# Performance work log

Hardware: AMD Instinct MI355X
Metric: run time of the kernel (lower is better)

## Reference

```python
import jax, jax.numpy as jnp
import numpy as np

EMB_DIM = 1024
N_HEAD = 16
HEAD_DIM = EMB_DIM // N_HEAD


def setup_inputs() -> dict:
    key = jax.random.key(0)
    k1, k2, k3, k4, k5 = jax.random.split(key, 5)
    x = jax.random.normal(k1, (4, 2048, EMB_DIM), dtype=jnp.float32)
    s = 1.0 / np.sqrt(EMB_DIM)
    W_qkv = jax.random.uniform(k2, (3 * EMB_DIM, EMB_DIM), minval=-s, maxval=s, dtype=jnp.float32)
    b_qkv = jax.random.uniform(k3, (3 * EMB_DIM,), minval=-s, maxval=s, dtype=jnp.float32)
    W_proj = jax.random.uniform(k4, (EMB_DIM, EMB_DIM), minval=-s, maxval=s, dtype=jnp.float32)
    b_proj = jax.random.uniform(k5, (EMB_DIM,), minval=-s, maxval=s, dtype=jnp.float32)
    return {"x": x, "W_qkv": W_qkv, "b_qkv": b_qkv, "W_proj": W_proj, "b_proj": b_proj}


def reference(x, W_qkv, b_qkv, W_proj, b_proj):
    B, S, E = x.shape
    H, D = N_HEAD, HEAD_DIM
    qkv = x @ W_qkv.T + b_qkv  # [B,S,3E]
    q, k, v = jnp.split(qkv, 3, axis=-1)
    # [B,S,E] -> [B,H,S,D]
    q = q.reshape(B, S, H, D).transpose(0, 2, 1, 3)
    k = k.reshape(B, S, H, D).transpose(0, 2, 1, 3)
    v = v.reshape(B, S, H, D).transpose(0, 2, 1, 3)
    scale = 1.0 / jnp.sqrt(jnp.asarray(D, dtype=x.dtype))
    scores = jnp.einsum('bhqd,bhkd->bhqk', q, k) * scale
    causal = jnp.tril(jnp.ones((S, S), dtype=bool))
    scores = jnp.where(causal, scores, jnp.asarray(-jnp.inf, dtype=scores.dtype))
    attn = jax.nn.softmax(scores, axis=-1)
    y = jnp.einsum('bhqk,bhkd->bhqd', attn, v)  # [B,H,S,D]
    y = y.transpose(0, 2, 1, 3).reshape(B, S, E)
    return y @ W_proj.T + b_proj
```

## Files before the change

kernel.cpp:

```cpp
#include <hip/hip_runtime.h>
#include <hip/hip_bf16.h>

typedef __attribute__((ext_vector_type(4))) float f32x4;
typedef __attribute__((ext_vector_type(8))) __bf16 bf16x8;
typedef __attribute__((ext_vector_type(4))) unsigned int u32x4;

#define EMB 1024
#define NHEAD 16
#define HDIM 64
#define SEQ 2048
#define BATCH 4
#define NTOK 8192

__device__ __forceinline__ unsigned short f2bf(float f) {
    unsigned int u = __builtin_bit_cast(unsigned int, f);
    u = (u + 0x7fffu + ((u >> 16) & 1u)) >> 16;
    return (unsigned short)u;
}

__device__ __forceinline__ unsigned int pack_bf2(float lo, float hi) {
    unsigned int a = __builtin_bit_cast(unsigned int, lo);
    unsigned int b = __builtin_bit_cast(unsigned int, hi);
    return ((a + 0x8000u) >> 16) | ((b + 0x8000u) & 0xffff0000u);
}

__device__ __forceinline__ unsigned long long pack_bf4(const f32x4 v) {
    unsigned long long lo = pack_bf2(v[0], v[1]);
    unsigned long long hi = pack_bf2(v[2], v[3]);
    return (hi << 32) | lo;
}

__device__ __forceinline__ void async_copy16(const ushort* g, ushort* l) {
    __builtin_amdgcn_global_load_lds(
        (const __attribute__((address_space(1))) void*)g,
        (__attribute__((address_space(3))) void*)l,
        16, 0, 0);
}

__global__ void cvt_f32_bf16(const float4* __restrict__ in, ushort* __restrict__ out, int n4) {
    int i = blockIdx.x * 256 + threadIdx.x;
    if (i < n4) {
        float4 v = in[i];
        ushort4 o;
        o.x = f2bf(v.x); o.y = f2bf(v.y); o.z = f2bf(v.z); o.w = f2bf(v.w);
        ((ushort4*)out)[i] = o;
    }
}

#define GEMM_STAGE(Asrc, Bsrc, m0, n0, kt)                                        \
    {                                                                             \
        _Pragma("unroll")                                                         \
        for (int j = 0; j < 2; ++j) {                                             \
            int row = wave * 32 + j * 16 + (lane >> 2);                           \
            int kc  = (lane & 3) ^ ((row >> 1) & 3);                              \
            async_copy16(Asrc + (size_t)(m0 + row) * EMB + kt + kc * 8,           \
                         As + (wave * 32 + j * 16) * 32);                         \
            async_copy16(Bsrc + (size_t)(n0 + row) * EMB + kt + kc * 8,           \
                         Bs + (wave * 32 + j * 16) * 32);                         \
        }                                                                         \
    }

#define GEMM_BODY(Asrc, Bsrc, m0, n0)                                             \
    f32x4 acc[4][4] = {};                                                         \
    for (int kt = 0; kt < EMB; kt += 32) {                                        \
        GEMM_STAGE(Asrc, Bsrc, m0, n0, kt)                                        \
        __syncthreads();                                                          \
        bf16x8 a[4], b[4];                                                        \
        _Pragma("unroll")                                                         \
        for (int i = 0; i < 4; ++i) {                                             \
            int r = wm + i * 16 + col;                                            \
            a[i] = *(const bf16x8*)&As[r * 32 + (quad ^ ((r >> 1) & 3)) * 8];     \
            int c = wn + i * 16 + col;                                            \
            b[i] = *(const bf16x8*)&Bs[c * 32 + (quad ^ ((c >> 1) & 3)) * 8];     \
        }                                                                         \
        _Pragma("unroll")                                                         \
        for (int i = 0; i < 4; ++i)                                               \
            _Pragma("unroll")                                                     \
            for (int j = 0; j < 4; ++j)                                           \
                acc[i][j] = __builtin_amdgcn_mfma_f32_16x16x32_bf16(              \
                    a[i], b[j], acc[i][j], 0, 0, 0);                              \
        __syncthreads();                                                         \
    }

__global__ __launch_bounds__(256) void gemm_qk(
    const ushort* __restrict__ A,
    const ushort* __restrict__ W,
    const float*  __restrict__ bias,
    ushort* __restrict__ Qb, ushort* __restrict__ Kb)
{
    __shared__ ushort As[128 * 32];
    __shared__ ushort Bs[128 * 32];
    const int tid  = threadIdx.x;
    const int lane = tid & 63;
    const int wave = tid >> 6;
    const int col  = lane & 15;
    const int quad = lane >> 4;
    const int m0 = blockIdx.x * 128;
    const int n0 = blockIdx.y * 128;
    const int wm = (wave >> 1) * 64;
    const int wn = (wave & 1) * 64;

    GEMM_BODY(A, W, m0, n0)

    #pragma unroll
    for (int i = 0; i < 4; ++i)
        #pragma unroll
        for (int j = 0; j < 4; ++j)
            #pragma unroll
            for (int r = 0; r < 4; ++r) {
                int m = m0 + wm + i * 16 + quad * 4 + r;
                int n = n0 + wn + j * 16 + col;
                float v = acc[i][j][r] + bias[n];
                unsigned short bv = f2bf(v);
                int e = n & 1023;
                int h = e >> 6, d = e & 63;
                int b = m >> 11, s = m & 2047;
                size_t bh = (size_t)(b * NHEAD + h);
                if (n < 1024) Qb[(bh * SEQ + s) * HDIM + d] = bv;
                else          Kb[(bh * SEQ + s) * HDIM + d] = bv;
            }
}

__global__ __launch_bounds__(256) void gemm_vt(
    const ushort* __restrict__ Wv,
    const ushort* __restrict__ X,
    const float*  __restrict__ bias,
    ushort* __restrict__ Vtx)
{
    __shared__ ushort As[128 * 32];
    __shared__ ushort Bs[128 * 32];
    const int tid  = threadIdx.x;
    const int lane = tid & 63;
    const int wave = tid >> 6;
    const int col  = lane & 15;
    const int quad = lane >> 4;
    const int m0 = blockIdx.x * 128;
    const int n0 = blockIdx.y * 128;
    const int wm = (wave >> 1) * 64;
    const int wn = (wave & 1) * 64;

    GEMM_BODY(Wv, X, m0, n0)

    #pragma unroll
    for (int i = 0; i < 4; ++i)
        #pragma unroll
        for (int j = 0; j < 4; ++j)
            #pragma unroll
            for (int r = 0; r < 4; ++r) {
                int m = m0 + wm + i * 16 + quad * 4 + r;
                int n = n0 + wn + j * 16 + col;
                Vtx[(size_t)m * NTOK + n] = f2bf(acc[i][j][r] + bias[m]);
            }
}

__global__ __launch_bounds__(256) void gemm_proj(
    const ushort* __restrict__ A,
    const ushort* __restrict__ W,
    const float*  __restrict__ bias,
    float* __restrict__ out)
{
    __shared__ ushort As[128 * 32];
    __shared__ ushort Bs[128 * 32];
    const int tid  = threadIdx.x;
    const int lane = tid & 63;
    const int wave = tid >> 6;
    const int col  = lane & 15;
    const int quad = lane >> 4;
    const int m0 = blockIdx.x * 128;
    const int n0 = blockIdx.y * 128;
    const int wm = (wave >> 1) * 64;
    const int wn = (wave & 1) * 64;

    GEMM_BODY(A, W, m0, n0)

    #pragma unroll
    for (int i = 0; i < 4; ++i)
        #pragma unroll
        for (int j = 0; j < 4; ++j)
            #pragma unroll
            for (int r = 0; r < 4; ++r) {
                int m = m0 + wm + i * 16 + quad * 4 + r;
                int n = n0 + wn + j * 16 + col;
                out[(size_t)m * EMB + n] = acc[i][j][r] + bias[n];
            }
}

__device__ __forceinline__ void attn_qtile(
    int qt, int b, int h, int lane, int wave,
    const ushort* __restrict__ Qh, const ushort* __restrict__ Kh,
    const ushort* __restrict__ Vh, ushort* __restrict__ Yb,
    ushort* __restrict__ Ks0, ushort* __restrict__ Ks1, ushort* __restrict__ Vs,
    ushort* __restrict__ Ps)
{
    const int col  = lane & 15;
    const int quad = lane >> 4;
    const int q0   = qt * 128 + wave * 32;
    const float SC = 0.125f * 1.44269504f;

    bf16x8 qf[2][2];
    #pragma unroll
    for (int g = 0; g < 2; ++g) {
        const ushort* qp = Qh + (size_t)(q0 + g * 16 + col) * HDIM;
        qf[g][0] = *(const bf16x8*)(qp + quad * 8);
        qf[g][1] = *(const bf16x8*)(qp + 32 + quad * 8);
    }

    ushort* Pw = Ps + wave * 4096;

    f32x4 o[2][4] = {};
    float lrun[2] = {0.f, 0.f};

    const int nk = qt + 1;
    for (int kt = 0; kt < nk; ++kt) {
        const int k0 = kt * 128;
        const bool last = (kt == nk - 1);

        {
            int srow = wave * 16 + (lane >> 2);
            #pragma unroll
            for (int rr = 0; rr < 2; ++rr) {
                int r = rr * 64 + srow;
                int kc = (lane & 3) ^ ((r >> 1) & 3);
                const ushort* src = Kh + (size_t)(k0 + r) * HDIM + kc * 8;
                async_copy16(src,      Ks0 + (rr * 64 + wave * 16) * 32);
                async_copy16(src + 32, Ks1 + (rr * 64 + wave * 16) * 32);
            }
            int kc = (lane & 3) ^ ((srow >> 1) & 3);
            const ushort* vsrc = Vh + (size_t)srow * NTOK + k0 + kc * 8;
            #pragma unroll
            for (int kq = 0; kq < 4; ++kq)
                async_copy16(vsrc + kq * 32, Vs + kq * 2048 + (wave * 16) * 32);
        }
        __syncthreads();

        f32x4 st[2][8];
        #pragma unroll
        for (int j = 0; j < 8; ++j) {
            int r = j * 16 + col;
            int q_ = (quad ^ ((r >> 1) & 3)) * 8;
            bf16x8 kf0 = *(const bf16x8*)&Ks0[r * 32 + q_];
            bf16x8 kf1 = *(const bf16x8*)&Ks1[r * 32 + q_];
            #pragma unroll
            for (int g = 0; g < 2; ++g) {
                f32x4 z = {0.f, 0.f, 0.f, 0.f};
                f32x4 t = __builtin_amdgcn_mfma_f32_16x16x32_bf16(kf0, qf[g][0], z, 0, 0, 0);
                st[g][j] = __builtin_amdgcn_mfma_f32_16x16x32_bf16(kf1, qf[g][1], t, 0, 0, 0);
            }
        }

        #pragma unroll
        for (int g = 0; g < 2; ++g) {
            int rowg = q0 + g * 16 + col;
            #pragma unroll
            for (int j = 0; j < 8; ++j)
                #pragma unroll
                for (int r = 0; r < 4; ++r) {
                    float pv = exp2f(st[g][j][r] * SC);
                    if (last) {
                        int c = k0 + j * 16 + quad * 4 + r;
                        pv = (c <= rowg) ? pv : 0.f;
                    }
                    st[g][j][r] = pv;
                    lrun[g] += pv;
                }
        }

        #pragma unroll
        for (int g = 0; g < 2; ++g)
            #pragma unroll
            for (int j = 0; j < 8; ++j) {
                int blk = 2 * j + (quad >> 1);
                *(unsigned long long*)&Pw[g * 2048 + col * 128 +
                                          ((blk ^ col) & 15) * 8 + (quad & 1) * 4]
                    = pack_bf4(st[g][j]);
            }
        bf16x8 pf[2][4];
        #pragma unroll
        for (int g = 0; g < 2; ++g)
            #pragma unroll
            for (int kq = 0; kq < 4; ++kq) {
                int blk = 4 * kq + quad;
                pf[g][kq] = *(const bf16x8*)&Pw[g * 2048 + col * 128 +
                                                ((blk ^ col) & 15) * 8];
            }

        #pragma unroll
        for (int dt = 0; dt < 4; ++dt) {
            int r = dt * 16 + col;
            int q_ = (quad ^ ((r >> 1) & 3)) * 8;
            #pragma unroll
            for (int kq = 0; kq < 4; ++kq) {
                bf16x8 vf = *(const bf16x8*)&Vs[kq * 2048 + r * 32 + q_];
                o[0][dt] = __builtin_amdgcn_mfma_f32_16x16x32_bf16(vf, pf[0][kq], o[0][dt], 0, 0, 0);
                o[1][dt] = __builtin_amdgcn_mfma_f32_16x16x32_bf16(vf, pf[1][kq], o[1][dt], 0, 0, 0);
            }
        }
        __syncthreads();
    }

    #pragma unroll
    for (int g = 0; g < 2; ++g) {
        float l = lrun[g];
        l += __shfl_xor(l, 16, 64);
        l += __shfl_xor(l, 32, 64);
        float inv = 1.f / l;
        int rowg = q0 + g * 16 + col;
        size_t rbase = ((size_t)(b * SEQ + rowg)) * EMB + h * HDIM + quad * 4;
        #pragma unroll
        for (int dt = 0; dt < 4; ++dt) {
            ushort4 s4;
            s4.x = f2bf(o[g][dt][0] * inv);
            s4.y = f2bf(o[g][dt][1] * inv);
            s4.z = f2bf(o[g][dt][2] * inv);
            s4.w = f2bf(o[g][dt][3] * inv);
            *(ushort4*)(Yb + rbase + dt * 16) = s4;
        }
    }
}

__global__ __launch_bounds__(256, 2) void attn(
    const ushort* __restrict__ Qb, const ushort* __restrict__ Kb,
    const ushort* __restrict__ Vtx, ushort* __restrict__ Yb)
{
    __shared__ ushort Ks0[128 * 32];
    __shared__ ushort Ks1[128 * 32];
    __shared__ ushort Vs[4 * 64 * 32];
    __shared__ __align__(16) ushort Ps[4 * 4096];
    const int lane = threadIdx.x & 63;
    const int wave = threadIdx.x >> 6;
    const int bh   = blockIdx.x & 63;
    const int pr   = blockIdx.x >> 6;

    const int b = bh >> 4, h = bh & 15;
    const ushort* Qh = Qb + (size_t)bh * SEQ * HDIM;
    const ushort* Kh = Kb + (size_t)bh * SEQ * HDIM;
    const ushort* Vh = Vtx + (size_t)(h * HDIM) * NTOK + b * SEQ;

    attn_qtile(15 - pr, b, h, lane, wave, Qh, Kh, Vh, Yb, Ks0, Ks1, Vs, Ps);
    __syncthreads();
    attn_qtile(pr,      b, h, lane, wave, Qh, Kh, Vh, Yb, Ks0, Ks1, Vs, Ps);
}

extern "C" void kernel_launch(void* const* d_in, const int* in_sizes, int n_in,
                              void* d_out, int out_size, void* d_ws, size_t ws_size,
                              hipStream_t stream) {
    const float* x      = (const float*)d_in[0];
    const float* W_qkv  = (const float*)d_in[1];
    const float* b_qkv  = (const float*)d_in[2];
    const float* W_proj = (const float*)d_in[3];
    const float* b_proj = (const float*)d_in[4];
    float* out = (float*)d_out;

    ushort* ws     = (ushort*)d_ws;
    ushort* Xb     = ws;
    ushort* Yb     = ws;
    ushort* Wqkvb  = ws + 8388608;
    ushort* Wprojb = ws + 11534336;
    ushort* Qb     = ws + 12582912;
    ushort* Kb     = ws + 20971520;
    ushort* Vtx    = ws + 29360128;

    cvt_f32_bf16<<<8192, 256, 0, stream>>>((const float4*)x,      Xb,     2097152);
    cvt_f32_bf16<<<3072, 256, 0, stream>>>((const float4*)W_qkv,  Wqkvb,  786432);
    cvt_f32_bf16<<<1024, 256, 0, stream>>>((const float4*)W_proj, Wprojb, 262144);

    gemm_qk<<<dim3(64, 16), 256, 0, stream>>>(Xb, Wqkvb, b_qkv, Qb, Kb);
    gemm_vt<<<dim3(8, 64), 256, 0, stream>>>(Wqkvb + (size_t)2048 * EMB, Xb,
                                             b_qkv + 2048, Vtx);
    attn<<<512, 256, 0, stream>>>(Qb, Kb, Vtx, Yb);
    gemm_proj<<<dim3(64, 8), 256, 0, stream>>>(Yb, Wprojb, b_proj, out);
}
```

Baseline: 269.5 us.

## Deepen GEMM K-step, shrink attention P buffer, raise occupancy, use hardware bf16 cvt

The GEMMs now stage 64 K-columns per barrier pair in two half buffers, halving the number of syncs and issuing more async loads per stage. The attention kernel splits the softmax exp loop into masked and unmasked paths and uses the raw hardware exp2. It reuses one P scratch slice per wave for both row groups, halving shared memory so that occupancy can be raised to 3 blocks per CU. bf16 packing switches to the compiler's native conversion, which rounds to nearest-even instead of rounding half up. The GEMMs use twice the LDS, and the tighter launch bounds may cause register spills.

```diff
diff --git a/kernel.cpp b/kernel.cpp
--- a/kernel.cpp
+++ b/kernel.cpp
@@ -18,16 +18,16 @@
     return (unsigned short)u;
 }
 
-__device__ __forceinline__ unsigned int pack_bf2(float lo, float hi) {
-    unsigned int a = __builtin_bit_cast(unsigned int, lo);
-    unsigned int b = __builtin_bit_cast(unsigned int, hi);
-    return ((a + 0x8000u) >> 16) | ((b + 0x8000u) & 0xffff0000u);
+__device__ __forceinline__ unsigned int cvt2_bf16(float lo, float hi) {
+    unsigned short a = __builtin_bit_cast(unsigned short, (__bf16)lo);
+    unsigned short b = __builtin_bit_cast(unsigned short, (__bf16)hi);
+    return (unsigned int)a | ((unsigned int)b << 16);
 }
 
 __device__ __forceinline__ unsigned long long pack_bf4(const f32x4 v) {
-    unsigned long long lo = pack_bf2(v[0], v[1]);
-    unsigned long long hi = pack_bf2(v[2], v[3]);
-    return (hi << 32) | lo;
+    unsigned long long lo = cvt2_bf16(v[0], v[1]);
+    unsigned long long hi = cvt2_bf16(v[2], v[3]);
+    return lo | (hi << 32);
 }
 
 __device__ __forceinline__ void async_copy16(const ushort* g, ushort* l) {
@@ -47,39 +47,46 @@
     }
 }
 
-#define GEMM_STAGE(Asrc, Bsrc, m0, n0, kt)                                        \
+#define GEMM_STAGE64(Asrc, Bsrc, m0, n0, kt)                                      \
     {                                                                             \
         _Pragma("unroll")                                                         \
         for (int j = 0; j < 2; ++j) {                                             \
             int row = wave * 32 + j * 16 + (lane >> 2);                           \
             int kc  = (lane & 3) ^ ((row >> 1) & 3);                              \
-            async_copy16(Asrc + (size_t)(m0 + row) * EMB + kt + kc * 8,           \
-                         As + (wave * 32 + j * 16) * 32);                         \
-            async_copy16(Bsrc + (size_t)(n0 + row) * EMB + kt + kc * 8,           \
-                         Bs + (wave * 32 + j * 16) * 32);                         \
+            const ushort* asrc = Asrc + (size_t)(m0 + row) * EMB + kt + kc * 8;   \
+            const ushort* bsrc = Bsrc + (size_t)(n0 + row) * EMB + kt + kc * 8;   \
+            async_copy16(asrc,      As0 + (wave * 32 + j * 16) * 32);             \
+            async_copy16(asrc + 32, As1 + (wave * 32 + j * 16) * 32);             \
+            async_copy16(bsrc,      Bs0 + (wave * 32 + j * 16) * 32);             \
+            async_copy16(bsrc + 32, Bs1 + (wave * 32 + j * 16) * 32);             \
         }                                                                         \
     }
 
-#define GEMM_BODY(Asrc, Bsrc, m0, n0)                                             \
+#define GEMM_BODY64(Asrc, Bsrc, m0, n0)                                           \
     f32x4 acc[4][4] = {};                                                         \
-    for (int kt = 0; kt < EMB; kt += 32) {                                        \
-        GEMM_STAGE(Asrc, Bsrc, m0, n0, kt)                                        \
+    for (int kt = 0; kt < EMB; kt += 64) {                                        \
+        GEMM_STAGE64(Asrc, Bsrc, m0, n0, kt)                                      \
         __syncthreads();                                                          \
-        bf16x8 a[4], b[4];                                                        \
         _Pragma("unroll")                                                         \
-        for (int i = 0; i < 4; ++i) {                                             \
-            int r = wm + i * 16 + col;                                            \
-            a[i] = *(const bf16x8*)&As[r * 32 + (quad ^ ((r >> 1) & 3)) * 8];     \
-            int c = wn + i * 16 + col;                                            \
-            b[i] = *(const bf16x8*)&Bs[c * 32 + (quad ^ ((c >> 1) & 3)) * 8];     \
+        for (int hf = 0; hf < 2; ++hf) {                                          \
+            const ushort* Ah = hf ? As1 : As0;                                    \
+            const ushort* Bh = hf ? Bs1 : Bs0;                                    \
+            bf16x8 a[4], b[4];                                                    \
+            _Pragma("unroll")                                                     \
+            for (int i = 0; i < 4; ++i) {                                         \
+                int r = wm + i * 16 + col;                                        \
+                a[i] = *(const bf16x8*)&Ah[r * 32 + (quad ^ ((r >> 1) & 3)) * 8]; \
+                int c = wn + i * 16 + col;                                        \
+                b[i] = *(const bf16x8*)&Bh[c * 32 + (quad ^ ((c >> 1) & 3)) * 8]; \
+            }                                                                     \
+            _Pragma("unroll")                                                     \
+            for (int i = 0; i < 4; ++i)                                           \
+                _Pragma("unroll")                                                 \
+                for (int j = 0; j < 4; ++j)                                       \
+                    acc[i][j] = __builtin_amdgcn_mfma_f32_16x16x32_bf16(          \
+                        a[i], b[j], acc[i][j], 0, 0, 0);                          \
         }                                                                         \
-        _Pragma("unroll")                                                         \
-        for (int i = 0; i < 4; ++i)                                               \
-            _Pragma("unroll")                                                     \
-            for (int j = 0; j < 4; ++j)                                           \
-                acc[i][j] = __builtin_amdgcn_mfma_f32_16x16x32_bf16(              \
-                    a[i], b[j], acc[i][j], 0, 0, 0);                              \
-        __syncthreads();                                                         \
+        __syncthreads();                                                          \
     }
 
 __global__ __launch_bounds__(256) void gemm_qk(
@@ -88,8 +95,10 @@
     const float*  __restrict__ bias,
     ushort* __restrict__ Qb, ushort* __restrict__ Kb)
 {
-    __shared__ ushort As[128 * 32];
-    __shared__ ushort Bs[128 * 32];
+    __shared__ ushort As0[128 * 32];
+    __shared__ ushort As1[128 * 32];
+    __shared__ ushort Bs0[128 * 32];
+    __shared__ ushort Bs1[128 * 32];
     const int tid  = threadIdx.x;
     const int lane = tid & 63;
     const int wave = tid >> 6;
@@ -100,7 +109,7 @@
     const int wm = (wave >> 1) * 64;
     const int wn = (wave & 1) * 64;
 
-    GEMM_BODY(A, W, m0, n0)
+    GEMM_BODY64(A, W, m0, n0)
 
     #pragma unroll
     for (int i = 0; i < 4; ++i)
@@ -127,8 +136,10 @@
     const float*  __restrict__ bias,
     ushort* __restrict__ Vtx)
 {
-    __shared__ ushort As[128 * 32];
-    __shared__ ushort Bs[128 * 32];
+    __shared__ ushort As0[128 * 32];
+    __shared__ ushort As1[128 * 32];
+    __shared__ ushort Bs0[128 * 32];
+    __shared__ ushort Bs1[128 * 32];
     const int tid  = threadIdx.x;
     const int lane = tid & 63;
     const int wave = tid >> 6;
@@ -139,7 +150,7 @@
     const int wm = (wave >> 1) * 64;
     const int wn = (wave & 1) * 64;
 
-    GEMM_BODY(Wv, X, m0, n0)
+    GEMM_BODY64(Wv, X, m0, n0)
 
     #pragma unroll
     for (int i = 0; i < 4; ++i)
@@ -159,8 +170,10 @@
     const float*  __restrict__ bias,
     float* __restrict__ out)
 {
-    __shared__ ushort As[128 * 32];
-    __shared__ ushort Bs[128 * 32];
+    __shared__ ushort As0[128 * 32];
+    __shared__ ushort As1[128 * 32];
+    __shared__ ushort Bs0[128 * 32];
+    __shared__ ushort Bs1[128 * 32];
     const int tid  = threadIdx.x;
     const int lane = tid & 63;
     const int wave = tid >> 6;
@@ -171,7 +184,7 @@
     const int wm = (wave >> 1) * 64;
     const int wn = (wave & 1) * 64;
 
-    GEMM_BODY(A, W, m0, n0)
+    GEMM_BODY64(A, W, m0, n0)
 
     #pragma unroll
     for (int i = 0; i < 4; ++i)
@@ -205,7 +218,7 @@
         qf[g][1] = *(const bf16x8*)(qp + 32 + quad * 8);
     }
 
-    ushort* Pw = Ps + wave * 4096;
+    ushort* Pw = Ps + wave * 2048;
 
     f32x4 o[2][4] = {};
     float lrun[2] = {0.f, 0.f};
@@ -248,41 +261,49 @@
             }
         }
 
-        #pragma unroll
-        for (int g = 0; g < 2; ++g) {
-            int rowg = q0 + g * 16 + col;
-            #pragma unroll
-            for (int j = 0; j < 8; ++j)
+        if (last) {
+            #pragma unroll
+            for (int g = 0; g < 2; ++g) {
+                int rowg = q0 + g * 16 + col;
                 #pragma unroll
-                for (int r = 0; r < 4; ++r) {
-                    float pv = exp2f(st[g][j][r] * SC);
-                    if (last) {
+                for (int j = 0; j < 8; ++j)
+                    #pragma unroll
+                    for (int r = 0; r < 4; ++r) {
+                        float pv = __builtin_amdgcn_exp2f(st[g][j][r] * SC);
                         int c = k0 + j * 16 + quad * 4 + r;
                         pv = (c <= rowg) ? pv : 0.f;
+                        st[g][j][r] = pv;
+                        lrun[g] += pv;
                     }
-                    st[g][j][r] = pv;
-                    lrun[g] += pv;
-                }
-        }
-
-        #pragma unroll
-        for (int g = 0; g < 2; ++g)
+            }
+        } else {
+            #pragma unroll
+            for (int g = 0; g < 2; ++g)
+                #pragma unroll
+                for (int j = 0; j < 8; ++j)
+                    #pragma unroll
+                    for (int r = 0; r < 4; ++r) {
+                        float pv = __builtin_amdgcn_exp2f(st[g][j][r] * SC);
+                        st[g][j][r] = pv;
+                        lrun[g] += pv;
+                    }
+        }
+
+        bf16x8 pf[2][4];
+        #pragma unroll
+        for (int g = 0; g < 2; ++g) {
             #pragma unroll
             for (int j = 0; j < 8; ++j) {
                 int blk = 2 * j + (quad >> 1);
-                *(unsigned long long*)&Pw[g * 2048 + col * 128 +
-                                          ((blk ^ col) & 15) * 8 + (quad & 1) * 4]
+                *(unsigned long long*)&Pw[col * 128 + ((blk ^ col) & 15) * 8 + (quad & 1) * 4]
                     = pack_bf4(st[g][j]);
             }
-        bf16x8 pf[2][4];
-        #pragma unroll
-        for (int g = 0; g < 2; ++g)
             #pragma unroll
             for (int kq = 0; kq < 4; ++kq) {
                 int blk = 4 * kq + quad;
-                pf[g][kq] = *(const bf16x8*)&Pw[g * 2048 + col * 128 +
-                                                ((blk ^ col) & 15) * 8];
-            }
+                pf[g][kq] = *(const bf16x8*)&Pw[col * 128 + ((blk ^ col) & 15) * 8];
+            }
+        }
 
         #pragma unroll
         for (int dt = 0; dt < 4; ++dt) {
@@ -318,14 +339,14 @@
     }
 }
 
-__global__ __launch_bounds__(256, 2) void attn(
+__global__ __launch_bounds__(256, 3) void attn(
     const ushort* __restrict__ Qb, const ushort* __restrict__ Kb,
     const ushort* __restrict__ Vtx, ushort* __restrict__ Yb)
 {
     __shared__ ushort Ks0[128 * 32];
     __shared__ ushort Ks1[128 * 32];
     __shared__ ushort Vs[4 * 64 * 32];
-    __shared__ __align__(16) ushort Ps[4 * 4096];
+    __shared__ __align__(16) ushort Ps[4 * 2048];
     const int lane = threadIdx.x & 63;
     const int wave = threadIdx.x >> 6;
     const int bh   = blockIdx.x & 63;
```

New measurement: 348.0 us. 1.29x slower.
